# Performance work log

Measured on AMD Instinct MI355X. Metric: run time of the kernel, lower is better.

## Reference

```python
import jax, jax.numpy as jnp
import numpy as np

U_NODES, V_NODES, N_EDGES = 100000, 50000, 2000000
F_DIM, G_DIM, H_DIM = 32, 32, 8
G_HIDDEN = (64, 32)
F_HIDDEN = (64, 32)
OUT_DIM = 1


def _linear_params(key, din, dout):
    kw, kb = jax.random.split(key)
    lim = 1.0 / np.sqrt(din)
    w = jax.random.uniform(kw, (din, dout), jnp.float32, -lim, lim)
    b = jax.random.uniform(kb, (dout,), jnp.float32, -lim, lim)
    return w, b


def setup_inputs() -> dict:
    key = jax.random.key(0)
    ks = jax.random.split(key, 10)
    u = jax.random.normal(ks[0], (U_NODES, F_DIM), jnp.float32)
    v = jax.random.normal(ks[1], (V_NODES, G_DIM), jnp.float32)
    e_vals = jax.random.normal(ks[2], (N_EDGES, H_DIM), jnp.float32)
    e_src = jax.random.randint(ks[3], (N_EDGES,), 0, V_NODES, jnp.int32)  # V-side index (indices[0])
    e_dst = jax.random.randint(ks[4], (N_EDGES,), 0, U_NODES, jnp.int32)  # U-side index (indices[1])
    g_w1, g_b1 = _linear_params(ks[5], F_DIM + G_DIM + H_DIM, G_HIDDEN[0])
    g_w2, g_b2 = _linear_params(ks[6], G_HIDDEN[0], G_HIDDEN[1])
    f_w1, f_b1 = _linear_params(ks[7], F_DIM + G_HIDDEN[1], F_HIDDEN[0])
    f_w2, f_b2 = _linear_params(ks[8], F_HIDDEN[0], F_HIDDEN[1])
    t_w, t_b = _linear_params(ks[9], F_HIDDEN[1], OUT_DIM)
    return {
        "u": u, "v": v, "e_vals": e_vals, "e_src": e_src, "e_dst": e_dst,
        "g_w1": g_w1, "g_b1": g_b1, "g_w2": g_w2, "g_b2": g_b2,
        "f_w1": f_w1, "f_b1": f_b1, "f_w2": f_w2, "f_b2": f_b2,
        "t_w": t_w, "t_b": t_b,
    }


def reference(u, v, e_vals, e_src, e_dst,
              g_w1, g_b1, g_w2, g_b2,
              f_w1, f_b1, f_w2, f_b2,
              t_w, t_b):
    # gather edge endpoint features -> g MLP (two Linear+ReLU layers)
    edge_in = jnp.concatenate([u[e_dst], v[e_src], e_vals], axis=-1)  # (E, F+G+H)
    h = jax.nn.relu(edge_in @ g_w1 + g_b1)
    h = jax.nn.relu(h @ g_w2 + g_b2)  # (E, D)
    # torch.sparse.sum over dim=-3 (V axis) == segment-sum by the U index
    agg = jax.ops.segment_sum(h, e_dst, num_segments=u.shape[0])  # (U, D)
    # f MLP on concat([u, agg])
    z = jax.nn.relu(jnp.concatenate([u, agg], axis=-1) @ f_w1 + f_b1)
    z = jax.nn.relu(z @ f_w2 + f_b2)
    # tail linear (no relu) + sigmoid
    return jax.nn.sigmoid(z @ t_w + t_b)  # (U, 1)
```

## Files before the change

kernel.cpp:

```cpp
#include <hip/hip_runtime.h>
#include <cstdint>
#include <cstddef>

#define U_NODES 100000
#define V_NODES 50000
#define N_EDGES 2000000


typedef _Float16 f16x8 __attribute__((ext_vector_type(8)));
typedef _Float16 f16x2 __attribute__((ext_vector_type(2)));
typedef float    f32x4 __attribute__((ext_vector_type(4)));

__device__ __forceinline__ void load8f(const float* __restrict__ p, float* x) {
    const float4* p4 = reinterpret_cast<const float4*>(p);
    float4 a = p4[0], b = p4[1];
    x[0]=a.x; x[1]=a.y; x[2]=a.z; x[3]=a.w;
    x[4]=b.x; x[5]=b.y; x[6]=b.z; x[7]=b.w;
}

__device__ __forceinline__ void load32f(const float* __restrict__ p, float* x) {
    #pragma unroll
    for (int q = 0; q < 4; ++q) load8f(p + 8*q, x + 8*q);
}

__device__ __forceinline__ unsigned pack_bf16x2(float a, float b) {
    unsigned ua = __float_as_uint(a);
    ua = (ua + 0x7FFFu + ((ua >> 16) & 1u)) >> 16;
    unsigned ub = __float_as_uint(b);
    ub = (ub + 0x7FFFu + ((ub >> 16) & 1u)) & 0xFFFF0000u;
    return ua | ub;
}

__device__ __forceinline__ unsigned pk16(float a, float b) {
    union { f16x2 h; unsigned u; } c;
    c.h[0] = (_Float16)a; c.h[1] = (_Float16)b;
    return c.u;
}
__device__ __forceinline__ float f16lo(unsigned w) {
    union { unsigned short u; _Float16 h; } c; c.u = (unsigned short)(w & 0xFFFFu);
    return (float)c.h;
}
__device__ __forceinline__ float f16hi(unsigned w) {
    union { unsigned short u; _Float16 h; } c; c.u = (unsigned short)(w >> 16);
    return (float)c.h;
}
__device__ __forceinline__ f16x8 as_f16x8(uint4 x) {
    union { uint4 u; f16x8 h; } c; c.u = x; return c.h;
}


__global__ __launch_bounds__(256) void proj_u_kernel(
    const float* __restrict__ u, const float* __restrict__ g_w1,
    float* __restrict__ A)
{
    int n = blockIdx.x * 256 + threadIdx.x;
    if (n >= U_NODES) return;
    float x[32];
    load32f(u + (size_t)n * 32, x);
    float acc[64];
    #pragma unroll
    for (int j = 0; j < 64; ++j) acc[j] = 0.f;
    #pragma unroll
    for (int i = 0; i < 32; ++i) {
        #pragma unroll
        for (int j = 0; j < 64; ++j) acc[j] += x[i] * g_w1[i*64 + j];
    }
    float4* Ap = reinterpret_cast<float4*>(A + (size_t)n * 64);
    #pragma unroll
    for (int q = 0; q < 16; ++q)
        Ap[q] = make_float4(acc[4*q], acc[4*q+1], acc[4*q+2], acc[4*q+3]);
}

__global__ __launch_bounds__(256) void proj_v_kernel(
    const float* __restrict__ v, const float* __restrict__ g_w1,
    const float* __restrict__ g_b1, float* __restrict__ B)
{
    int n = blockIdx.x * 256 + threadIdx.x;
    if (n >= V_NODES) return;
    float x[32];
    load32f(v + (size_t)n * 32, x);
    float acc[64];
    #pragma unroll
    for (int j = 0; j < 64; ++j) acc[j] = g_b1[j];
    #pragma unroll
    for (int i = 0; i < 32; ++i) {
        #pragma unroll
        for (int j = 0; j < 64; ++j) acc[j] += x[i] * g_w1[(32+i)*64 + j];
    }
    float4* Bp = reinterpret_cast<float4*>(B + (size_t)n * 64);
    #pragma unroll
    for (int q = 0; q < 16; ++q)
        Bp[q] = make_float4(acc[4*q], acc[4*q+1], acc[4*q+2], acc[4*q+3]);
}


__global__ __launch_bounds__(256) void rank_kernel(
    const int* __restrict__ e_dst, int* __restrict__ deg, int* __restrict__ rank)
{
    int e = blockIdx.x * 256 + threadIdx.x;
    if (e >= N_EDGES) return;
    rank[e] = atomicAdd(&deg[e_dst[e]], 1);
}

__global__ __launch_bounds__(256) void scan_block_kernel(
    const int* __restrict__ deg, int* __restrict__ off, int* __restrict__ aux, int n)
{
    __shared__ int s[256];
    int tid = threadIdx.x;
    int i = blockIdx.x * 256 + tid;
    int x = (i < n) ? deg[i] : 0;
    s[tid] = x;
    __syncthreads();
    #pragma unroll
    for (int o = 1; o < 256; o <<= 1) {
        int t = (tid >= o) ? s[tid - o] : 0;
        __syncthreads();
        s[tid] += t;
        __syncthreads();
    }
    if (i < n) off[i + 1] = s[tid];
    if (tid == 255) aux[blockIdx.x] = s[255];
}

__global__ __launch_bounds__(512) void scan_aux_kernel(int* __restrict__ aux, int nA)
{
    __shared__ int s[512];
    int tid = threadIdx.x;
    int x = (tid < nA) ? aux[tid] : 0;
    s[tid] = x;
    __syncthreads();
    #pragma unroll
    for (int o = 1; o < 512; o <<= 1) {
        int t = (tid >= o) ? s[tid - o] : 0;
        __syncthreads();
        s[tid] += t;
        __syncthreads();
    }
    if (tid < nA) aux[tid] = s[tid] - x;
}

__global__ __launch_bounds__(256) void scan_add_kernel(
    int* __restrict__ off, const int* __restrict__ aux, int n)
{
    int i = blockIdx.x * 256 + threadIdx.x;
    if (i == 0) off[0] = 0;
    if (i < n) off[i + 1] += aux[i >> 8];
}

__global__ __launch_bounds__(256) void scatter_kernel(
    const int* __restrict__ e_dst, const int* __restrict__ off,
    const int* __restrict__ rank, int* __restrict__ sorted_eid)
{
    int e = blockIdx.x * 256 + threadIdx.x;
    if (e >= N_EDGES) return;
    int d = e_dst[e];
    sorted_eid[off[d] + rank[e]] = e;
}

__global__ __launch_bounds__(256) void permute_pack_kernel(
    const int* __restrict__ e_dst, const int* __restrict__ e_src,
    const int* __restrict__ rank, const int* __restrict__ off,
    const float* __restrict__ e_vals, unsigned* __restrict__ epk)
{
    int e = blockIdx.x * 256 + threadIdx.x;
    if (e >= N_EDGES) return;
    int d = e_dst[e];
    int pos = off[d] + rank[e];
    float ev[8];
    load8f(e_vals + (size_t)e * 8, ev);
    uint4 w0;
    w0.x = (unsigned)d;
    w0.y = (unsigned)e_src[e];
    w0.z = pk16(ev[0], ev[1]);
    w0.w = pk16(ev[2], ev[3]);
    uint2 w1;
    w1.x = pk16(ev[4], ev[5]);
    w1.y = pk16(ev[6], ev[7]);
    unsigned* dst = epk + (size_t)pos * 8;
    *reinterpret_cast<uint4*>(dst)     = w0;
    *reinterpret_cast<uint2*>(dst + 4) = w1;
}


template <bool HAS_A>
__global__ __launch_bounds__(256) void edge_mfma_kernel(
    const float* __restrict__ A, const float* __restrict__ B,
    const float* __restrict__ u, const unsigned* __restrict__ epk,
    const float* __restrict__ g_w1, const float* __restrict__ g_w2,
    const float* __restrict__ g_b2, float* __restrict__ agg)
{
    __shared__ unsigned s_h1[256 * 36];
    __shared__ unsigned s_w2[32 * 33];
    __shared__ int s_d[256];
    __shared__ int s_heads[256];
    __shared__ int s_cnt, s_prevd, s_nextd;

    const int tid = threadIdx.x;
    const long p = (long)blockIdx.x * 256 + tid;

    if (tid == 0) {
        s_cnt = 0;
        long pprev = (long)blockIdx.x * 256 - 1;
        s_prevd = (pprev < 0) ? -2 : (int)epk[(size_t)pprev * 8];
        long pnext = (long)blockIdx.x * 256 + 256;
        s_nextd = (pnext >= N_EDGES) ? -2 : (int)epk[(size_t)pnext * 8];
    }

    #pragma unroll
    for (int i = 0; i < 4; ++i) {
        int idx = tid + i * 256;
        int kp = idx >> 5, n = idx & 31;
        s_w2[kp * 33 + n] = pk16(g_w2[(2*kp)*32 + n], g_w2[(2*kp+1)*32 + n]);
    }

    int d = -1;
    if (p < N_EDGES) {
        const unsigned* ep = epk + (size_t)p * 8;
        uint4 w0 = *reinterpret_cast<const uint4*>(ep);
        uint2 w1 = *reinterpret_cast<const uint2*>(ep + 4);
        d = (int)w0.x;
        int s = (int)w0.y;

        float h1[64];
        if constexpr (HAS_A) {
            const float4* Ap = reinterpret_cast<const float4*>(A + (size_t)d * 64);
            #pragma unroll
            for (int q = 0; q < 16; ++q) {
                float4 a = Ap[q];
                h1[4*q+0] = a.x; h1[4*q+1] = a.y; h1[4*q+2] = a.z; h1[4*q+3] = a.w;
            }
        } else {
            #pragma unroll
            for (int j = 0; j < 64; ++j) h1[j] = 0.f;
            float x[32];
            load32f(u + (size_t)d * 32, x);
            #pragma unroll
            for (int i = 0; i < 32; ++i) {
                #pragma unroll
                for (int j = 0; j < 64; ++j) h1[j] += x[i] * g_w1[i*64 + j];
            }
        }
        {
            const float4* Bp = reinterpret_cast<const float4*>(B + (size_t)s * 64);
            #pragma unroll
            for (int q = 0; q < 16; ++q) {
                float4 b = Bp[q];
                h1[4*q+0] += b.x; h1[4*q+1] += b.y; h1[4*q+2] += b.z; h1[4*q+3] += b.w;
            }
        }
        float ev[8];
        ev[0]=f16lo(w0.z); ev[1]=f16hi(w0.z); ev[2]=f16lo(w0.w); ev[3]=f16hi(w0.w);
        ev[4]=f16lo(w1.x); ev[5]=f16hi(w1.x); ev[6]=f16lo(w1.y); ev[7]=f16hi(w1.y);
        #pragma unroll
        for (int i = 0; i < 8; ++i) {
            #pragma unroll
            for (int j = 0; j < 64; ++j) h1[j] += ev[i] * g_w1[(64+i)*64 + j];
        }
        #pragma unroll
        for (int j = 0; j < 64; ++j) h1[j] = fmaxf(h1[j], 0.f);

        #pragma unroll
        for (int q = 0; q < 8; ++q) {
            uint4 w;
            w.x = pk16(h1[8*q+0], h1[8*q+1]);
            w.y = pk16(h1[8*q+2], h1[8*q+3]);
            w.z = pk16(h1[8*q+4], h1[8*q+5]);
            w.w = pk16(h1[8*q+6], h1[8*q+7]);
            *reinterpret_cast<uint4*>(&s_h1[tid*36 + 4*q]) = w;
        }
    }
    s_d[tid] = d;
    __syncthreads();

    if (p < N_EDGES) {
        int prevd = (tid == 0) ? s_prevd : s_d[tid - 1];
        bool true_head = (prevd != d);
        bool is_head = (tid == 0) || true_head;
        if (is_head) {
            int idx = atomicAdd(&s_cnt, 1);
            s_heads[idx] = tid | (true_head ? 0x10000 : 0);
        }
    }

    const int lane = tid & 63;
    const int wb   = (tid >> 6) * 64;
    const int lg   = lane >> 4;
    const int lm   = lane & 15;

    f32x4 acc[4][2];
    #pragma unroll
    for (int mt = 0; mt < 4; ++mt) {
        #pragma unroll
        for (int nt = 0; nt < 2; ++nt) {
            acc[mt][nt][0] = 0.f; acc[mt][nt][1] = 0.f;
            acc[mt][nt][2] = 0.f; acc[mt][nt][3] = 0.f;
        }
    }
    #pragma unroll
    for (int kt = 0; kt < 2; ++kt) {
        uint4 bf0, bf1;
        {
            int kp = kt*16 + lg*4;
            bf0.x = s_w2[(kp+0)*33 + lm];      bf1.x = s_w2[(kp+0)*33 + 16 + lm];
            bf0.y = s_w2[(kp+1)*33 + lm];      bf1.y = s_w2[(kp+1)*33 + 16 + lm];
            bf0.z = s_w2[(kp+2)*33 + lm];      bf1.z = s_w2[(kp+2)*33 + 16 + lm];
            bf0.w = s_w2[(kp+3)*33 + lm];      bf1.w = s_w2[(kp+3)*33 + 16 + lm];
        }
        f16x8 b0 = as_f16x8(bf0), b1 = as_f16x8(bf1);
        #pragma unroll
        for (int mt = 0; mt < 4; ++mt) {
            uint4 av = *reinterpret_cast<const uint4*>(
                &s_h1[(wb + mt*16 + lm)*36 + kt*16 + lg*4]);
            f16x8 a = as_f16x8(av);
            acc[mt][0] = __builtin_amdgcn_mfma_f32_16x16x32_f16(a, b0, acc[mt][0], 0, 0, 0);
            acc[mt][1] = __builtin_amdgcn_mfma_f32_16x16x32_f16(a, b1, acc[mt][1], 0, 0, 0);
        }
    }
    float b2a = g_b2[lm];
    float b2b = g_b2[16 + lm];
    __syncthreads();

    float* h2f = reinterpret_cast<float*>(s_h1);
    #pragma unroll
    for (int mt = 0; mt < 4; ++mt) {
        #pragma unroll
        for (int r = 0; r < 4; ++r) {
            int row = wb + mt*16 + lg*4 + r;
            h2f[row*36 + lm]      = fmaxf(acc[mt][0][r] + b2a, 0.f);
            h2f[row*36 + 16 + lm] = fmaxf(acc[mt][1][r] + b2b, 0.f);
        }
    }
    __syncthreads();

    const int nseg = s_cnt;
    const int next_d = s_nextd;
    for (int w = tid; w < nseg * 16; w += 256) {
        int seg = w >> 4, cp = w & 15;
        int ent = s_heads[seg];
        int h = ent & 0xFFFF;
        bool thead = (ent & 0x10000) != 0;
        int dd = s_d[h];
        float s0 = 0.f, s1 = 0.f;
        int r = h;
        while (r < 256 && s_d[r] == dd) {
            s0 += h2f[r*36 + 2*cp];
            s1 += h2f[r*36 + 2*cp + 1];
            ++r;
        }
        bool end_complete = (r < 256) || (next_d != dd);
        float* dst = agg + (size_t)dd * 32 + 2 * cp;
        if (thead && end_complete) {
            *reinterpret_cast<float2*>(dst) = make_float2(s0, s1);
        } else {
            atomicAdd(dst + 0, s0);
            atomicAdd(dst + 1, s1);
        }
    }
}


template <bool HAS_A, bool HAS_B>
__global__ __launch_bounds__(256) void edge_sorted_kernel(
    const float* __restrict__ A, const float* __restrict__ B,
    const float* __restrict__ u, const float* __restrict__ v,
    const float* __restrict__ e_vals, const int* __restrict__ e_src,
    const int* __restrict__ e_dst, const int* __restrict__ seid,
    const float* __restrict__ g_w1, const float* __restrict__ g_b1,
    const float* __restrict__ g_w2, const float* __restrict__ g_b2,
    float* __restrict__ agg)
{
    __shared__ unsigned lds_h[256][17];
    __shared__ int lds_d[256];
    __shared__ int lds_heads[256];
    __shared__ int lds_cnt;
    __shared__ int lds_prev_d, lds_next_d;

    const int tid = threadIdx.x;
    const long p = (long)blockIdx.x * 256 + tid;

    if (tid == 0) {
        lds_cnt = 0;
        long pprev = (long)blockIdx.x * 256 - 1;
        lds_prev_d = (pprev < 0) ? -2 : e_dst[seid[pprev]];
        long pnext = (long)blockIdx.x * 256 + 256;
        lds_next_d = (pnext >= N_EDGES) ? -2 : e_dst[seid[pnext]];
    }

    int d = -1;
    if (p < N_EDGES) {
        int eid = seid[p];
        d = e_dst[eid];
        int s = e_src[eid];

        float h1[64];
        if constexpr (HAS_A) {
            const float4* Ap = reinterpret_cast<const float4*>(A + (size_t)d * 64);
            #pragma unroll
            for (int q = 0; q < 16; ++q) {
                float4 a = Ap[q];
                h1[4*q+0] = a.x; h1[4*q+1] = a.y; h1[4*q+2] = a.z; h1[4*q+3] = a.w;
            }
        } else {
            #pragma unroll
            for (int j = 0; j < 64; ++j) h1[j] = 0.f;
            float x[32];
            load32f(u + (size_t)d * 32, x);
            #pragma unroll
            for (int i = 0; i < 32; ++i) {
                #pragma unroll
                for (int j = 0; j < 64; ++j) h1[j] += x[i] * g_w1[i*64 + j];
            }
        }
        if constexpr (HAS_B) {
            const float4* Bp = reinterpret_cast<const float4*>(B + (size_t)s * 64);
            #pragma unroll
            for (int q = 0; q < 16; ++q) {
                float4 b = Bp[q];
                h1[4*q+0] += b.x; h1[4*q+1] += b.y; h1[4*q+2] += b.z; h1[4*q+3] += b.w;
            }
        } else {
            #pragma unroll
            for (int j = 0; j < 64; ++j) h1[j] += g_b1[j];
            float x[32];
            load32f(v + (size_t)s * 32, x);
            #pragma unroll
            for (int i = 0; i < 32; ++i) {
                #pragma unroll
                for (int j = 0; j < 64; ++j) h1[j] += x[i] * g_w1[(32+i)*64 + j];
            }
        }
        float ev[8];
        load8f(e_vals + (size_t)eid * 8, ev);
        #pragma unroll
        for (int i = 0; i < 8; ++i) {
            #pragma unroll
            for (int j = 0; j < 64; ++j) h1[j] += ev[i] * g_w1[(64+i)*64 + j];
        }
        #pragma unroll
        for (int j = 0; j < 64; ++j) h1[j] = fmaxf(h1[j], 0.f);

        float h2[32];
        #pragma unroll
        for (int k = 0; k < 32; ++k) h2[k] = g_b2[k];
        #pragma unroll
        for (int i = 0; i < 64; ++i) {
            #pragma unroll
            for (int k = 0; k < 32; ++k) h2[k] += h1[i] * g_w2[i*32 + k];
        }
        #pragma unroll
        for (int cp = 0; cp < 16; ++cp)
            lds_h[tid][cp] = pack_bf16x2(fmaxf(h2[2*cp], 0.f), fmaxf(h2[2*cp+1], 0.f));
    }
    lds_d[tid] = d;
    __syncthreads();

    if (p < N_EDGES) {
        int prevd = (tid == 0) ? lds_prev_d : lds_d[tid - 1];
        bool true_head = (prevd != d);
        bool is_head = (tid == 0) || true_head;
        if (is_head) {
            int idx = atomicAdd(&lds_cnt, 1);
            lds_heads[idx] = tid | (true_head ? 0x10000 : 0);
        }
    }
    __syncthreads();

    const int nseg = lds_cnt;
    const int next_d = lds_next_d;
    for (int w = tid; w < nseg * 16; w += 256) {
        int seg = w >> 4, cp = w & 15;
        int ent = lds_heads[seg];
        int h = ent & 0xFFFF;
        bool thead = (ent & 0x10000) != 0;
        int dd = lds_d[h];
        float s0 = 0.f, s1 = 0.f;
        int r = h;
        while (r < 256 && lds_d[r] == dd) {
            unsigned x = lds_h[r][cp];
            s0 += __uint_as_float(x << 16);
            s1 += __uint_as_float(x & 0xFFFF0000u);
            ++r;
        }
        bool end_complete = (r < 256) || (next_d != dd);
        float* dst = agg + (size_t)dd * 32 + 2 * cp;
        if (thead && end_complete) {
            *reinterpret_cast<float2*>(dst) = make_float2(s0, s1);
        } else {
            atomicAdd(dst + 0, s0);
            atomicAdd(dst + 1, s1);
        }
    }
}


__global__ __launch_bounds__(256) void node_kernel(
    const float* __restrict__ u, const float* __restrict__ agg,
    const float* __restrict__ f_w1, const float* __restrict__ f_b1,
    const float* __restrict__ f_w2, const float* __restrict__ f_b2,
    const float* __restrict__ t_w, const float* __restrict__ t_b,
    float* __restrict__ out)
{
    int n = blockIdx.x * 256 + threadIdx.x;
    if (n >= U_NODES) return;
    float x[64];
    load32f(u   + (size_t)n * 32, x);
    load32f(agg + (size_t)n * 32, x + 32);
    float z1[64];
    #pragma unroll
    for (int j = 0; j < 64; ++j) z1[j] = f_b1[j];
    #pragma unroll
    for (int i = 0; i < 64; ++i) {
        #pragma unroll
        for (int j = 0; j < 64; ++j) z1[j] += x[i] * f_w1[i*64 + j];
    }
    #pragma unroll
    for (int j = 0; j < 64; ++j) z1[j] = fmaxf(z1[j], 0.f);
    float z2[32];
    #pragma unroll
    for (int k = 0; k < 32; ++k) z2[k] = f_b2[k];
    #pragma unroll
    for (int j = 0; j < 64; ++j) {
        #pragma unroll
        for (int k = 0; k < 32; ++k) z2[k] += z1[j] * f_w2[j*32 + k];
    }
    #pragma unroll
    for (int k = 0; k < 32; ++k) z2[k] = fmaxf(z2[k], 0.f);
    float o = t_b[0];
    #pragma unroll
    for (int k = 0; k < 32; ++k) o += z2[k] * t_w[k];
    out[n] = 1.f / (1.f + expf(-o));
}


__global__ __launch_bounds__(256) void edge_direct_kernel(
    const float* __restrict__ u, const float* __restrict__ v,
    const float* __restrict__ e_vals, const int* __restrict__ e_src,
    const int* __restrict__ e_dst, const float* __restrict__ g_w1,
    const float* __restrict__ g_b1, const float* __restrict__ g_w2,
    const float* __restrict__ g_b2, float* __restrict__ agg)
{
    int e = blockIdx.x * 256 + threadIdx.x;
    if (e >= N_EDGES) return;
    int d = e_dst[e];
    int s = e_src[e];
    float x[72];
    load32f(u + (size_t)d * 32, x);
    load32f(v + (size_t)s * 32, x + 32);
    load8f(e_vals + (size_t)e * 8, x + 64);
    float h1[64];
    #pragma unroll
    for (int j = 0; j < 64; ++j) h1[j] = g_b1[j];
    #pragma unroll
    for (int i = 0; i < 72; ++i) {
        #pragma unroll
        for (int j = 0; j < 64; ++j) h1[j] += x[i] * g_w1[i*64 + j];
    }
    #pragma unroll
    for (int j = 0; j < 64; ++j) h1[j] = fmaxf(h1[j], 0.f);
    float acc2[32];
    #pragma unroll
    for (int k = 0; k < 32; ++k) acc2[k] = g_b2[k];
    #pragma unroll
    for (int i = 0; i < 64; ++i) {
        #pragma unroll
        for (int k = 0; k < 32; ++k) acc2[k] += h1[i] * g_w2[i*32 + k];
    }
    float* aggp = agg + (size_t)d * 32;
    #pragma unroll
    for (int k = 0; k < 32; ++k) atomicAdd(aggp + k, fmaxf(acc2[k], 0.f));
}


static inline size_t align256(size_t x) { return (x + 255) & ~(size_t)255; }

extern "C" void kernel_launch(void* const* d_in, const int* in_sizes, int n_in,
                              void* d_out, int out_size, void* d_ws, size_t ws_size,
                              hipStream_t stream) {
    const float* u      = (const float*)d_in[0];
    const float* v      = (const float*)d_in[1];
    const float* e_vals = (const float*)d_in[2];
    const int*   e_src  = (const int*)  d_in[3];
    const int*   e_dst  = (const int*)  d_in[4];
    const float* g_w1   = (const float*)d_in[5];
    const float* g_b1   = (const float*)d_in[6];
    const float* g_w2   = (const float*)d_in[7];
    const float* g_b2   = (const float*)d_in[8];
    const float* f_w1   = (const float*)d_in[9];
    const float* f_b1   = (const float*)d_in[10];
    const float* f_w2   = (const float*)d_in[11];
    const float* f_b2   = (const float*)d_in[12];
    const float* t_w    = (const float*)d_in[13];
    const float* t_b    = (const float*)d_in[14];
    float* out = (float*)d_out;

    char* wsc = (char*)d_ws;
    const int nChunks = (U_NODES + 255) / 256;
    const int eBlocks = (N_EDGES + 255) / 256;

    const size_t degB  = align256((size_t)U_NODES * 4);
    const size_t offB  = align256((size_t)(U_NODES + 1) * 4);
    const size_t auxB  = align256((size_t)nChunks * 4);
    const size_t aggB  = align256((size_t)U_NODES * 32 * 4);
    const size_t e4B   = align256((size_t)N_EDGES * 4);
    const size_t epkB  = align256((size_t)N_EDGES * 32);
    const size_t bB    = align256((size_t)V_NODES * 64 * 4);
    const size_t aB    = align256((size_t)U_NODES * 64 * 4);

    size_t o = 0;
    size_t oDeg = o; o += degB;
    size_t oOff = o; o += offB;
    size_t oAux = o; o += auxB;
    size_t oAgg = o; o += aggB;
    size_t baseNeed = o;

    size_t oEp = o;  o += epkB;
    size_t oBn = o;  o += bB;
    size_t needT2r = o + e4B;
    size_t oAn = o;  o += aB;
    size_t needT1 = o;

    size_t o3 = baseNeed;
    size_t oSeid = o3; o3 += e4B;
    size_t needT4 = o3 + e4B;
    size_t oB3 = o3;   o3 += bB;
    size_t oA3 = o3;   o3 += aB;
    size_t needT3 = o3;

    int* deg   = (int*)(wsc + oDeg);
    int* off   = (int*)(wsc + oOff);
    int* aux   = (int*)(wsc + oAux);
    float* agg = (float*)(wsc + oAgg);

    if (ws_size >= needT2r) {
        const bool hasA = (ws_size >= needT1);
        unsigned* epk = (unsigned*)(wsc + oEp);
        float* B   = (float*)(wsc + oBn);
        float* A   = hasA ? (float*)(wsc + oAn) : nullptr;
        int* rank  = hasA ? (int*)A : (int*)(wsc + oAn);

        hipMemsetAsync(deg, 0, (size_t)U_NODES * 4, stream);
        hipMemsetAsync(agg, 0, (size_t)U_NODES * 32 * 4, stream);

        rank_kernel<<<eBlocks, 256, 0, stream>>>(e_dst, deg, rank);
        scan_block_kernel<<<nChunks, 256, 0, stream>>>(deg, off, aux, U_NODES);
        scan_aux_kernel<<<1, 512, 0, stream>>>(aux, nChunks);
        scan_add_kernel<<<nChunks, 256, 0, stream>>>(off, aux, U_NODES);
        permute_pack_kernel<<<eBlocks, 256, 0, stream>>>(e_dst, e_src, rank, off,
                                                         e_vals, epk);
        proj_v_kernel<<<(V_NODES + 255) / 256, 256, 0, stream>>>(v, g_w1, g_b1, B);
        if (hasA) {
            proj_u_kernel<<<(U_NODES + 255) / 256, 256, 0, stream>>>(u, g_w1, A);
            edge_mfma_kernel<true><<<eBlocks, 256, 0, stream>>>(
                A, B, u, epk, g_w1, g_w2, g_b2, agg);
        } else {
            edge_mfma_kernel<false><<<eBlocks, 256, 0, stream>>>(
                nullptr, B, u, epk, g_w1, g_w2, g_b2, agg);
        }
        node_kernel<<<(U_NODES + 255) / 256, 256, 0, stream>>>(
            u, agg, f_w1, f_b1, f_w2, f_b2, t_w, t_b, out);
    } else if (ws_size >= needT4) {
        const bool hasAB = (ws_size >= needT3);
        int* seid = (int*)(wsc + oSeid);
        float* B = hasAB ? (float*)(wsc + oB3) : nullptr;
        float* A = hasAB ? (float*)(wsc + oA3) : nullptr;
        int* rank = hasAB ? (int*)A : (int*)(wsc + oSeid + e4B);

        hipMemsetAsync(deg, 0, (size_t)U_NODES * 4, stream);
        hipMemsetAsync(agg, 0, (size_t)U_NODES * 32 * 4, stream);

        rank_kernel<<<eBlocks, 256, 0, stream>>>(e_dst, deg, rank);
        scan_block_kernel<<<nChunks, 256, 0, stream>>>(deg, off, aux, U_NODES);
        scan_aux_kernel<<<1, 512, 0, stream>>>(aux, nChunks);
        scan_add_kernel<<<nChunks, 256, 0, stream>>>(off, aux, U_NODES);
        scatter_kernel<<<eBlocks, 256, 0, stream>>>(e_dst, off, rank, seid);

        if (hasAB) {
            proj_v_kernel<<<(V_NODES + 255) / 256, 256, 0, stream>>>(v, g_w1, g_b1, B);
            proj_u_kernel<<<(U_NODES + 255) / 256, 256, 0, stream>>>(u, g_w1, A);
            edge_sorted_kernel<true, true><<<eBlocks, 256, 0, stream>>>(
                A, B, u, v, e_vals, e_src, e_dst, seid, g_w1, g_b1, g_w2, g_b2, agg);
        } else {
            edge_sorted_kernel<false, false><<<eBlocks, 256, 0, stream>>>(
                nullptr, nullptr, u, v, e_vals, e_src, e_dst, seid,
                g_w1, g_b1, g_w2, g_b2, agg);
        }
        node_kernel<<<(U_NODES + 255) / 256, 256, 0, stream>>>(
            u, agg, f_w1, f_b1, f_w2, f_b2, t_w, t_b, out);
    } else {
        float* agg0 = (float*)wsc;
        hipMemsetAsync(agg0, 0, (size_t)U_NODES * 32 * 4, stream);
        edge_direct_kernel<<<eBlocks, 256, 0, stream>>>(
            u, v, e_vals, e_src, e_dst, g_w1, g_b1, g_w2, g_b2, agg0);
        node_kernel<<<(U_NODES + 255) / 256, 256, 0, stream>>>(
            u, agg0, f_w1, f_b1, f_w2, f_b2, t_w, t_b, out);
    }
}
```

Baseline: 422.5 us.

## Replace per-node counting sort with 64-node bucket sort and block-local aggregation

Replaces the per-destination atomic rank, full U-sized scan and permute with a coarse bucket sort: 64-node buckets are histogrammed in shared memory per 1024-thread block, then packed in block-local order. The edge kernel now runs one block per bucket, computes the first layer per-lane with fdot2 for the edge features, runs layer two on MFMA, and accumulates into shared-memory agg with LDS atomics before one coalesced write. This removes global atomics, the agg memset and the segment-head logic. In exchange, bucket sizes vary, each block's loop length depends on its edge count, and shared-memory atomic contention rises on hot nodes.

```diff
diff --git a/kernel.cpp b/kernel.cpp
--- a/kernel.cpp
+++ b/kernel.cpp
@@ -5,6 +5,13 @@
 #define U_NODES 100000
 #define V_NODES 50000
 #define N_EDGES 2000000
+#define UBLKS ((U_NODES + 255) / 256)
+#define VBLKS ((V_NODES + 255) / 256)
+
+#define BNODES 64
+#define NBUK ((U_NODES + BNODES - 1) / BNODES)
+#define HB 128
+#define EPB ((N_EDGES + HB - 1) / HB)
 
 
 typedef _Float16 f16x8 __attribute__((ext_vector_type(8)));
@@ -48,6 +55,15 @@
     union { uint4 u; f16x8 h; } c; c.u = x; return c.h;
 }
 
+__device__ __forceinline__ float fdot2f(unsigned a, unsigned b, float c) {
+#if defined(__has_builtin) && __has_builtin(__builtin_amdgcn_fdot2)
+    union { unsigned u; f16x2 h; } ca, cb; ca.u = a; cb.u = b;
+    return __builtin_amdgcn_fdot2(ca.h, cb.h, c, false);
+#else
+    return c + f16lo(a)*f16lo(b) + f16hi(a)*f16hi(b);
+#endif
+}
+
 
 __global__ __launch_bounds__(256) void proj_u_kernel(
     const float* __restrict__ u, const float* __restrict__ g_w1,
@@ -94,12 +110,23 @@
 }
 
 
-__global__ __launch_bounds__(256) void rank_kernel(
-    const int* __restrict__ e_dst, int* __restrict__ deg, int* __restrict__ rank)
-{
-    int e = blockIdx.x * 256 + threadIdx.x;
-    if (e >= N_EDGES) return;
-    rank[e] = atomicAdd(&deg[e_dst[e]], 1);
+__global__ __launch_bounds__(1024) void bucket_hist_kernel(
+    const int* __restrict__ e_dst, int* __restrict__ bucketcnt,
+    int* __restrict__ blockbase)
+{
+    __shared__ int hist[NBUK];
+    const int tid = threadIdx.x, blk = blockIdx.x;
+    for (int i = tid; i < NBUK; i += 1024) hist[i] = 0;
+    __syncthreads();
+    int e0 = blk * EPB;
+    int e1 = e0 + EPB; if (e1 > N_EDGES) e1 = N_EDGES;
+    for (int e = e0 + tid; e < e1; e += 1024)
+        atomicAdd(&hist[e_dst[e] >> 6], 1);
+    __syncthreads();
+    for (int b = tid; b < NBUK; b += 1024) {
+        int c = hist[b];
+        blockbase[blk * NBUK + b] = c ? atomicAdd(&bucketcnt[b], c) : 0;
+    }
 }
 
 __global__ __launch_bounds__(256) void scan_block_kernel(
@@ -147,64 +174,79 @@
     if (i < n) off[i + 1] += aux[i >> 8];
 }
 
-__global__ __launch_bounds__(256) void scatter_kernel(
-    const int* __restrict__ e_dst, const int* __restrict__ off,
-    const int* __restrict__ rank, int* __restrict__ sorted_eid)
-{
-    int e = blockIdx.x * 256 + threadIdx.x;
-    if (e >= N_EDGES) return;
-    int d = e_dst[e];
-    sorted_eid[off[d] + rank[e]] = e;
-}
-
-__global__ __launch_bounds__(256) void permute_pack_kernel(
+__global__ __launch_bounds__(1024) void bucket_pack_kernel(
     const int* __restrict__ e_dst, const int* __restrict__ e_src,
-    const int* __restrict__ rank, const int* __restrict__ off,
-    const float* __restrict__ e_vals, unsigned* __restrict__ epk)
-{
-    int e = blockIdx.x * 256 + threadIdx.x;
-    if (e >= N_EDGES) return;
-    int d = e_dst[e];
-    int pos = off[d] + rank[e];
-    float ev[8];
-    load8f(e_vals + (size_t)e * 8, ev);
-    uint4 w0;
-    w0.x = (unsigned)d;
-    w0.y = (unsigned)e_src[e];
-    w0.z = pk16(ev[0], ev[1]);
-    w0.w = pk16(ev[2], ev[3]);
-    uint2 w1;
-    w1.x = pk16(ev[4], ev[5]);
-    w1.y = pk16(ev[6], ev[7]);
-    unsigned* dst = epk + (size_t)pos * 8;
-    *reinterpret_cast<uint4*>(dst)     = w0;
-    *reinterpret_cast<uint2*>(dst + 4) = w1;
-}
-
-
-template <bool HAS_A>
-__global__ __launch_bounds__(256) void edge_mfma_kernel(
+    const float* __restrict__ e_vals, const int* __restrict__ bucket_off,
+    const int* __restrict__ blockbase, unsigned* __restrict__ epk)
+{
+    __shared__ int cur[NBUK];
+    __shared__ int base[NBUK];
+    const int tid = threadIdx.x, blk = blockIdx.x;
+    for (int i = tid; i < NBUK; i += 1024) {
+        cur[i] = 0;
+        base[i] = bucket_off[i] + blockbase[blk * NBUK + i];
+    }
+    __syncthreads();
+    int e0 = blk * EPB;
+    int e1 = e0 + EPB; if (e1 > N_EDGES) e1 = N_EDGES;
+    for (int e = e0 + tid; e < e1; e += 1024) {
+        int d = e_dst[e];
+        int b = d >> 6;
+        int lr = atomicAdd(&cur[b], 1);
+        int pos = base[b] + lr;
+        float ev[8];
+        load8f(e_vals + (size_t)e * 8, ev);
+        uint4 w0;
+        w0.x = (unsigned)d;
+        w0.y = (unsigned)e_src[e];
+        w0.z = pk16(ev[0], ev[1]);
+        w0.w = pk16(ev[2], ev[3]);
+        uint2 w1;
+        w1.x = pk16(ev[4], ev[5]);
+        w1.y = pk16(ev[6], ev[7]);
+        unsigned* dst = epk + (size_t)pos * 8;
+        *reinterpret_cast<uint4*>(dst)     = w0;
+        *reinterpret_cast<uint2*>(dst + 4) = w1;
+    }
+}
+
+
+__device__ __forceinline__ void load_recs_b(
+    const unsigned* __restrict__ epk, int beg, int cnt, int t, int wv, int lm,
+    int* dM, int* sM, unsigned (*evp)[4])
+{
+    #pragma unroll
+    for (int mt = 0; mt < 4; ++mt) {
+        int rel = t*256 + wv*64 + mt*16 + lm;
+        if (rel < cnt) {
+            const unsigned* ep = epk + (size_t)(beg + rel) * 8;
+            uint4 w0 = *reinterpret_cast<const uint4*>(ep);
+            uint2 w1 = *reinterpret_cast<const uint2*>(ep + 4);
+            dM[mt] = (int)w0.x; sM[mt] = (int)w0.y;
+            evp[mt][0] = w0.z; evp[mt][1] = w0.w; evp[mt][2] = w1.x; evp[mt][3] = w1.y;
+        } else {
+            dM[mt] = -1; sM[mt] = 0;
+            evp[mt][0] = evp[mt][1] = evp[mt][2] = evp[mt][3] = 0;
+        }
+    }
+}
+
+__global__ __launch_bounds__(256) void edge_agg_kernel(
     const float* __restrict__ A, const float* __restrict__ B,
-    const float* __restrict__ u, const unsigned* __restrict__ epk,
+    const unsigned* __restrict__ epk, const int* __restrict__ bucket_off,
     const float* __restrict__ g_w1, const float* __restrict__ g_w2,
     const float* __restrict__ g_b2, float* __restrict__ agg)
 {
-    __shared__ unsigned s_h1[256 * 36];
+    __shared__ float s_agg[BNODES * 33];
     __shared__ unsigned s_w2[32 * 33];
-    __shared__ int s_d[256];
-    __shared__ int s_heads[256];
-    __shared__ int s_cnt, s_prevd, s_nextd;
+    __shared__ __align__(16) unsigned s_w1e[4 * 64];
+    __shared__ int s_dl[2][256];
 
     const int tid = threadIdx.x;
-    const long p = (long)blockIdx.x * 256 + tid;
-
-    if (tid == 0) {
-        s_cnt = 0;
-        long pprev = (long)blockIdx.x * 256 - 1;
-        s_prevd = (pprev < 0) ? -2 : (int)epk[(size_t)pprev * 8];
-        long pnext = (long)blockIdx.x * 256 + 256;
-        s_nextd = (pnext >= N_EDGES) ? -2 : (int)epk[(size_t)pnext * 8];
-    }
+    const int bk  = blockIdx.x;
+    const int beg = bucket_off[bk];
+    const int cnt = bucket_off[bk + 1] - beg;
+    const int node0 = bk * BNODES;
 
     #pragma unroll
     for (int i = 0; i < 4; ++i) {
@@ -212,152 +254,183 @@
         int kp = idx >> 5, n = idx & 31;
         s_w2[kp * 33 + n] = pk16(g_w2[(2*kp)*32 + n], g_w2[(2*kp+1)*32 + n]);
     }
-
-    int d = -1;
-    if (p < N_EDGES) {
-        const unsigned* ep = epk + (size_t)p * 8;
-        uint4 w0 = *reinterpret_cast<const uint4*>(ep);
-        uint2 w1 = *reinterpret_cast<const uint2*>(ep + 4);
-        d = (int)w0.x;
-        int s = (int)w0.y;
-
-        float h1[64];
-        if constexpr (HAS_A) {
-            const float4* Ap = reinterpret_cast<const float4*>(A + (size_t)d * 64);
-            #pragma unroll
-            for (int q = 0; q < 16; ++q) {
-                float4 a = Ap[q];
-                h1[4*q+0] = a.x; h1[4*q+1] = a.y; h1[4*q+2] = a.z; h1[4*q+3] = a.w;
-            }
-        } else {
-            #pragma unroll
-            for (int j = 0; j < 64; ++j) h1[j] = 0.f;
-            float x[32];
-            load32f(u + (size_t)d * 32, x);
-            #pragma unroll
-            for (int i = 0; i < 32; ++i) {
+    {
+        int i2 = tid >> 6, c = tid & 63;
+        s_w1e[i2 * 64 + c] = pk16(g_w1[(64 + 2*i2)*64 + c], g_w1[(64 + 2*i2 + 1)*64 + c]);
+    }
+    for (int i = tid; i < BNODES * 33; i += 256) s_agg[i] = 0.f;
+
+    const int wv   = tid >> 6;
+    const int lane = tid & 63;
+    const int lm   = lane & 15;
+    const int lg   = lane >> 4;
+    const float b2a = g_b2[lm], b2b = g_b2[16 + lm];
+
+    const int nt = (cnt + 255) >> 8;
+    int dC[4], sC[4]; unsigned evC[4][4];
+    if (nt > 0) load_recs_b(epk, beg, cnt, 0, wv, lm, dC, sC, evC);
+    __syncthreads();
+
+    for (int t = 0; t < nt; ++t) {
+        uint4 afr[4][2];
+        #pragma unroll
+        for (int kt = 0; kt < 2; ++kt) {
+            float acc[4][8];
+            #pragma unroll
+            for (int mt = 0; mt < 4; ++mt) {
+                if (dC[mt] >= 0) {
+                    const float4* Ap = reinterpret_cast<const float4*>(A + (size_t)dC[mt]*64 + kt*32 + lg*8);
+                    const float4* Bp = reinterpret_cast<const float4*>(B + (size_t)sC[mt]*64 + kt*32 + lg*8);
+                    float4 a0 = Ap[0], a1 = Ap[1], b0 = Bp[0], b1 = Bp[1];
+                    acc[mt][0] = a0.x + b0.x; acc[mt][1] = a0.y + b0.y;
+                    acc[mt][2] = a0.z + b0.z; acc[mt][3] = a0.w + b0.w;
+                    acc[mt][4] = a1.x + b1.x; acc[mt][5] = a1.y + b1.y;
+                    acc[mt][6] = a1.z + b1.z; acc[mt][7] = a1.w + b1.w;
+                } else {
+                    #pragma unroll
+                    for (int j = 0; j < 8; ++j) acc[mt][j] = 0.f;
+                }
+            }
+            #pragma unroll
+            for (int i2 = 0; i2 < 4; ++i2) {
+                uint4 wA = *reinterpret_cast<const uint4*>(&s_w1e[i2*64 + kt*32 + lg*8]);
+                uint4 wB = *reinterpret_cast<const uint4*>(&s_w1e[i2*64 + kt*32 + lg*8 + 4]);
                 #pragma unroll
-                for (int j = 0; j < 64; ++j) h1[j] += x[i] * g_w1[i*64 + j];
-            }
-        }
-        {
-            const float4* Bp = reinterpret_cast<const float4*>(B + (size_t)s * 64);
-            #pragma unroll
-            for (int q = 0; q < 16; ++q) {
-                float4 b = Bp[q];
-                h1[4*q+0] += b.x; h1[4*q+1] += b.y; h1[4*q+2] += b.z; h1[4*q+3] += b.w;
-            }
-        }
-        float ev[8];
-        ev[0]=f16lo(w0.z); ev[1]=f16hi(w0.z); ev[2]=f16lo(w0.w); ev[3]=f16hi(w0.w);
-        ev[4]=f16lo(w1.x); ev[5]=f16hi(w1.x); ev[6]=f16lo(w1.y); ev[7]=f16hi(w1.y);
-        #pragma unroll
-        for (int i = 0; i < 8; ++i) {
-            #pragma unroll
-            for (int j = 0; j < 64; ++j) h1[j] += ev[i] * g_w1[(64+i)*64 + j];
-        }
-        #pragma unroll
-        for (int j = 0; j < 64; ++j) h1[j] = fmaxf(h1[j], 0.f);
-
-        #pragma unroll
-        for (int q = 0; q < 8; ++q) {
-            uint4 w;
-            w.x = pk16(h1[8*q+0], h1[8*q+1]);
-            w.y = pk16(h1[8*q+2], h1[8*q+3]);
-            w.z = pk16(h1[8*q+4], h1[8*q+5]);
-            w.w = pk16(h1[8*q+6], h1[8*q+7]);
-            *reinterpret_cast<uint4*>(&s_h1[tid*36 + 4*q]) = w;
-        }
-    }
-    s_d[tid] = d;
-    __syncthreads();
-
-    if (p < N_EDGES) {
-        int prevd = (tid == 0) ? s_prevd : s_d[tid - 1];
-        bool true_head = (prevd != d);
-        bool is_head = (tid == 0) || true_head;
-        if (is_head) {
-            int idx = atomicAdd(&s_cnt, 1);
-            s_heads[idx] = tid | (true_head ? 0x10000 : 0);
-        }
-    }
-
-    const int lane = tid & 63;
-    const int wb   = (tid >> 6) * 64;
-    const int lg   = lane >> 4;
-    const int lm   = lane & 15;
-
-    f32x4 acc[4][2];
-    #pragma unroll
-    for (int mt = 0; mt < 4; ++mt) {
-        #pragma unroll
-        for (int nt = 0; nt < 2; ++nt) {
-            acc[mt][nt][0] = 0.f; acc[mt][nt][1] = 0.f;
-            acc[mt][nt][2] = 0.f; acc[mt][nt][3] = 0.f;
-        }
-    }
-    #pragma unroll
-    for (int kt = 0; kt < 2; ++kt) {
-        uint4 bf0, bf1;
-        {
+                for (int mt = 0; mt < 4; ++mt) {
+                    unsigned e2 = evC[mt][i2];
+                    acc[mt][0] = fdot2f(e2, wA.x, acc[mt][0]);
+                    acc[mt][1] = fdot2f(e2, wA.y, acc[mt][1]);
+                    acc[mt][2] = fdot2f(e2, wA.z, acc[mt][2]);
+                    acc[mt][3] = fdot2f(e2, wA.w, acc[mt][3]);
+                    acc[mt][4] = fdot2f(e2, wB.x, acc[mt][4]);
+                    acc[mt][5] = fdot2f(e2, wB.y, acc[mt][5]);
+                    acc[mt][6] = fdot2f(e2, wB.z, acc[mt][6]);
+                    acc[mt][7] = fdot2f(e2, wB.w, acc[mt][7]);
+                }
+            }
+            #pragma unroll
+            for (int mt = 0; mt < 4; ++mt) {
+                uint4 w;
+                w.x = pk16(fmaxf(acc[mt][0], 0.f), fmaxf(acc[mt][1], 0.f));
+                w.y = pk16(fmaxf(acc[mt][2], 0.f), fmaxf(acc[mt][3], 0.f));
+                w.z = pk16(fmaxf(acc[mt][4], 0.f), fmaxf(acc[mt][5], 0.f));
+                w.w = pk16(fmaxf(acc[mt][6], 0.f), fmaxf(acc[mt][7], 0.f));
+                afr[mt][kt] = w;
+            }
+        }
+
+        f32x4 mac[4][2];
+        #pragma unroll
+        for (int mt = 0; mt < 4; ++mt) {
+            #pragma unroll
+            for (int nt2 = 0; nt2 < 2; ++nt2) {
+                mac[mt][nt2][0] = 0.f; mac[mt][nt2][1] = 0.f;
+                mac[mt][nt2][2] = 0.f; mac[mt][nt2][3] = 0.f;
+            }
+        }
+        #pragma unroll
+        for (int kt = 0; kt < 2; ++kt) {
+            uint4 bf0, bf1;
             int kp = kt*16 + lg*4;
             bf0.x = s_w2[(kp+0)*33 + lm];      bf1.x = s_w2[(kp+0)*33 + 16 + lm];
             bf0.y = s_w2[(kp+1)*33 + lm];      bf1.y = s_w2[(kp+1)*33 + 16 + lm];
             bf0.z = s_w2[(kp+2)*33 + lm];      bf1.z = s_w2[(kp+2)*33 + 16 + lm];
             bf0.w = s_w2[(kp+3)*33 + lm];      bf1.w = s_w2[(kp+3)*33 + 16 + lm];
-        }
-        f16x8 b0 = as_f16x8(bf0), b1 = as_f16x8(bf1);
+            f16x8 b0 = as_f16x8(bf0), b1 = as_f16x8(bf1);
+            #pragma unroll
+            for (int mt = 0; mt < 4; ++mt) {
+                f16x8 a = as_f16x8(afr[mt][kt]);
+                mac[mt][0] = __builtin_amdgcn_mfma_f32_16x16x32_f16(a, b0, mac[mt][0], 0, 0, 0);
+                mac[mt][1] = __builtin_amdgcn_mfma_f32_16x16x32_f16(a, b1, mac[mt][1], 0, 0, 0);
+            }
+        }
+
+        if (lg == 0) {
+            #pragma unroll
+            for (int mt = 0; mt < 4; ++mt) s_dl[t & 1][wv*64 + mt*16 + lm] = dC[mt];
+        }
+        __syncthreads();
+
+        if (t + 1 < nt) load_recs_b(epk, beg, cnt, t + 1, wv, lm, dC, sC, evC);
+
         #pragma unroll
         for (int mt = 0; mt < 4; ++mt) {
-            uint4 av = *reinterpret_cast<const uint4*>(
-                &s_h1[(wb + mt*16 + lm)*36 + kt*16 + lg*4]);
-            f16x8 a = as_f16x8(av);
-            acc[mt][0] = __builtin_amdgcn_mfma_f32_16x16x32_f16(a, b0, acc[mt][0], 0, 0, 0);
-            acc[mt][1] = __builtin_amdgcn_mfma_f32_16x16x32_f16(a, b1, acc[mt][1], 0, 0, 0);
-        }
-    }
-    float b2a = g_b2[lm];
-    float b2b = g_b2[16 + lm];
-    __syncthreads();
-
-    float* h2f = reinterpret_cast<float*>(s_h1);
-    #pragma unroll
-    for (int mt = 0; mt < 4; ++mt) {
-        #pragma unroll
-        for (int r = 0; r < 4; ++r) {
-            int row = wb + mt*16 + lg*4 + r;
-            h2f[row*36 + lm]      = fmaxf(acc[mt][0][r] + b2a, 0.f);
-            h2f[row*36 + 16 + lm] = fmaxf(acc[mt][1][r] + b2b, 0.f);
-        }
-    }
-    __syncthreads();
-
-    const int nseg = s_cnt;
-    const int next_d = s_nextd;
-    for (int w = tid; w < nseg * 16; w += 256) {
-        int seg = w >> 4, cp = w & 15;
-        int ent = s_heads[seg];
-        int h = ent & 0xFFFF;
-        bool thead = (ent & 0x10000) != 0;
-        int dd = s_d[h];
-        float s0 = 0.f, s1 = 0.f;
-        int r = h;
-        while (r < 256 && s_d[r] == dd) {
-            s0 += h2f[r*36 + 2*cp];
-            s1 += h2f[r*36 + 2*cp + 1];
-            ++r;
-        }
-        bool end_complete = (r < 256) || (next_d != dd);
-        float* dst = agg + (size_t)dd * 32 + 2 * cp;
-        if (thead && end_complete) {
-            *reinterpret_cast<float2*>(dst) = make_float2(s0, s1);
-        } else {
-            atomicAdd(dst + 0, s0);
-            atomicAdd(dst + 1, s1);
-        }
-    }
-}
-
+            #pragma unroll
+            for (int r = 0; r < 4; ++r) {
+                int dd = s_dl[t & 1][wv*64 + mt*16 + lg*4 + r];
+                if (dd >= 0) {
+                    int loc = (dd & (BNODES - 1)) * 33;
+                    atomicAdd(&s_agg[loc + lm],      fmaxf(mac[mt][0][r] + b2a, 0.f));
+                    atomicAdd(&s_agg[loc + 16 + lm], fmaxf(mac[mt][1][r] + b2b, 0.f));
+                }
+            }
+        }
+    }
+    __syncthreads();
+
+    for (int i = tid; i < BNODES * 32; i += 256) {
+        int n = node0 + (i >> 5);
+        if (n < U_NODES) agg[(size_t)n * 32 + (i & 31)] = s_agg[(i >> 5) * 33 + (i & 31)];
+    }
+}
+
+
+__global__ __launch_bounds__(256) void node_kernel(
+    const float* __restrict__ u, const float* __restrict__ agg,
+    const float* __restrict__ f_w1, const float* __restrict__ f_b1,
+    const float* __restrict__ f_w2, const float* __restrict__ f_b2,
+    const float* __restrict__ t_w, const float* __restrict__ t_b,
+    float* __restrict__ out)
+{
+    int n = blockIdx.x * 256 + threadIdx.x;
+    if (n >= U_NODES) return;
+    float x[64];
+    load32f(u   + (size_t)n * 32, x);
+    load32f(agg + (size_t)n * 32, x + 32);
+    float z1[64];
+    #pragma unroll
+    for (int j = 0; j < 64; ++j) z1[j] = f_b1[j];
+    #pragma unroll
+    for (int i = 0; i < 64; ++i) {
+        #pragma unroll
+        for (int j = 0; j < 64; ++j) z1[j] += x[i] * f_w1[i*64 + j];
+    }
+    #pragma unroll
+    for (int j = 0; j < 64; ++j) z1[j] = fmaxf(z1[j], 0.f);
+    float z2[32];
+    #pragma unroll
+    for (int k = 0; k < 32; ++k) z2[k] = f_b2[k];
+    #pragma unroll
+    for (int j = 0; j < 64; ++j) {
+        #pragma unroll
+        for (int k = 0; k < 32; ++k) z2[k] += z1[j] * f_w2[j*32 + k];
+    }
+    #pragma unroll
+    for (int k = 0; k < 32; ++k) z2[k] = fmaxf(z2[k], 0.f);
+    float o = t_b[0];
+    #pragma unroll
+    for (int k = 0; k < 32; ++k) o += z2[k] * t_w[k];
+    out[n] = 1.f / (1.f + expf(-o));
+}
+
+
+__global__ __launch_bounds__(256) void rank_kernel(
+    const int* __restrict__ e_dst, int* __restrict__ deg, int* __restrict__ rank)
+{
+    int e = blockIdx.x * 256 + threadIdx.x;
+    if (e >= N_EDGES) return;
+    rank[e] = atomicAdd(&deg[e_dst[e]], 1);
+}
+
+__global__ __launch_bounds__(256) void scatter_kernel(
+    const int* __restrict__ e_dst, const int* __restrict__ off,
+    const int* __restrict__ rank, int* __restrict__ sorted_eid)
+{
+    int e = blockIdx.x * 256 + threadIdx.x;
+    if (e >= N_EDGES) return;
+    int d = e_dst[e];
+    sorted_eid[off[d] + rank[e]] = e;
+}
 
 template <bool HAS_A, bool HAS_B>
 __global__ __launch_bounds__(256) void edge_sorted_kernel(
@@ -491,46 +564,6 @@
         }
     }
 }
-
-
-__global__ __launch_bounds__(256) void node_kernel(
-    const float* __restrict__ u, const float* __restrict__ agg,
-    const float* __restrict__ f_w1, const float* __restrict__ f_b1,
-    const float* __restrict__ f_w2, const float* __restrict__ f_b2,
-    const float* __restrict__ t_w, const float* __restrict__ t_b,
-    float* __restrict__ out)
-{
-    int n = blockIdx.x * 256 + threadIdx.x;
-    if (n >= U_NODES) return;
-    float x[64];
-    load32f(u   + (size_t)n * 32, x);
-    load32f(agg + (size_t)n * 32, x + 32);
-    float z1[64];
-    #pragma unroll
-    for (int j = 0; j < 64; ++j) z1[j] = f_b1[j];
-    #pragma unroll
-    for (int i = 0; i < 64; ++i) {
-        #pragma unroll
-        for (int j = 0; j < 64; ++j) z1[j] += x[i] * f_w1[i*64 + j];
-    }
-    #pragma unroll
-    for (int j = 0; j < 64; ++j) z1[j] = fmaxf(z1[j], 0.f);
-    float z2[32];
-    #pragma unroll
-    for (int k = 0; k < 32; ++k) z2[k] = f_b2[k];
-    #pragma unroll
-    for (int j = 0; j < 64; ++j) {
-        #pragma unroll
-        for (int k = 0; k < 32; ++k) z2[k] += z1[j] * f_w2[j*32 + k];
-    }
-    #pragma unroll
-    for (int k = 0; k < 32; ++k) z2[k] = fmaxf(z2[k], 0.f);
-    float o = t_b[0];
-    #pragma unroll
-    for (int k = 0; k < 32; ++k) o += z2[k] * t_w[k];
-    out[n] = 1.f / (1.f + expf(-o));
-}
-
 
 __global__ __launch_bounds__(256) void edge_direct_kernel(
     const float* __restrict__ u, const float* __restrict__ v,
@@ -594,73 +627,76 @@
     float* out = (float*)d_out;
 
     char* wsc = (char*)d_ws;
-    const int nChunks = (U_NODES + 255) / 256;
     const int eBlocks = (N_EDGES + 255) / 256;
-
-    const size_t degB  = align256((size_t)U_NODES * 4);
-    const size_t offB  = align256((size_t)(U_NODES + 1) * 4);
-    const size_t auxB  = align256((size_t)nChunks * 4);
+    const int nChunksB = (NBUK + 255) / 256;
+
+    const size_t bcB   = align256((size_t)NBUK * 4);
+    const size_t boB   = align256((size_t)(NBUK + 1) * 4);
+    const size_t auxB  = align256((size_t)nChunksB * 4);
+    const size_t bbB   = align256((size_t)HB * NBUK * 4);
     const size_t aggB  = align256((size_t)U_NODES * 32 * 4);
-    const size_t e4B   = align256((size_t)N_EDGES * 4);
     const size_t epkB  = align256((size_t)N_EDGES * 32);
     const size_t bB    = align256((size_t)V_NODES * 64 * 4);
     const size_t aB    = align256((size_t)U_NODES * 64 * 4);
+    const size_t e4B   = align256((size_t)N_EDGES * 4);
 
     size_t o = 0;
-    size_t oDeg = o; o += degB;
-    size_t oOff = o; o += offB;
+    size_t oBc  = o; o += bcB;
+    size_t oBo  = o; o += boB;
     size_t oAux = o; o += auxB;
+    size_t oBb  = o; o += bbB;
     size_t oAgg = o; o += aggB;
-    size_t baseNeed = o;
-
-    size_t oEp = o;  o += epkB;
-    size_t oBn = o;  o += bB;
-    size_t needT2r = o + e4B;
-    size_t oAn = o;  o += aB;
-    size_t needT1 = o;
-
-    size_t o3 = baseNeed;
+    size_t oEp  = o; o += epkB;
+    size_t oBn  = o; o += bB;
+    size_t oAn  = o; o += aB;
+    size_t needNew = o;
+
+    const size_t degB = align256((size_t)U_NODES * 4);
+    const size_t offB = align256((size_t)(U_NODES + 1) * 4);
+    const int nChunksU = (U_NODES + 255) / 256;
+    const size_t auxUB = align256((size_t)nChunksU * 4);
+    size_t o3 = 0;
+    size_t oDeg3 = o3; o3 += degB;
+    size_t oOff3 = o3; o3 += offB;
+    size_t oAux3 = o3; o3 += auxUB;
+    size_t oAgg3 = o3; o3 += aggB;
     size_t oSeid = o3; o3 += e4B;
     size_t needT4 = o3 + e4B;
     size_t oB3 = o3;   o3 += bB;
     size_t oA3 = o3;   o3 += aB;
     size_t needT3 = o3;
 
-    int* deg   = (int*)(wsc + oDeg);
-    int* off   = (int*)(wsc + oOff);
-    int* aux   = (int*)(wsc + oAux);
-    float* agg = (float*)(wsc + oAgg);
-
-    if (ws_size >= needT2r) {
-        const bool hasA = (ws_size >= needT1);
-        unsigned* epk = (unsigned*)(wsc + oEp);
-        float* B   = (float*)(wsc + oBn);
-        float* A   = hasA ? (float*)(wsc + oAn) : nullptr;
-        int* rank  = hasA ? (int*)A : (int*)(wsc + oAn);
-
-        hipMemsetAsync(deg, 0, (size_t)U_NODES * 4, stream);
-        hipMemsetAsync(agg, 0, (size_t)U_NODES * 32 * 4, stream);
-
-        rank_kernel<<<eBlocks, 256, 0, stream>>>(e_dst, deg, rank);
-        scan_block_kernel<<<nChunks, 256, 0, stream>>>(deg, off, aux, U_NODES);
-        scan_aux_kernel<<<1, 512, 0, stream>>>(aux, nChunks);
-        scan_add_kernel<<<nChunks, 256, 0, stream>>>(off, aux, U_NODES);
-        permute_pack_kernel<<<eBlocks, 256, 0, stream>>>(e_dst, e_src, rank, off,
-                                                         e_vals, epk);
-        proj_v_kernel<<<(V_NODES + 255) / 256, 256, 0, stream>>>(v, g_w1, g_b1, B);
-        if (hasA) {
-            proj_u_kernel<<<(U_NODES + 255) / 256, 256, 0, stream>>>(u, g_w1, A);
-            edge_mfma_kernel<true><<<eBlocks, 256, 0, stream>>>(
-                A, B, u, epk, g_w1, g_w2, g_b2, agg);
-        } else {
-            edge_mfma_kernel<false><<<eBlocks, 256, 0, stream>>>(
-                nullptr, B, u, epk, g_w1, g_w2, g_b2, agg);
-        }
-        node_kernel<<<(U_NODES + 255) / 256, 256, 0, stream>>>(
+    if (ws_size >= needNew) {
+        int* bucketcnt = (int*)(wsc + oBc);
+        int* bucketoff = (int*)(wsc + oBo);
+        int* aux       = (int*)(wsc + oAux);
+        int* blockbase = (int*)(wsc + oBb);
+        float* agg     = (float*)(wsc + oAgg);
+        unsigned* epk  = (unsigned*)(wsc + oEp);
+        float* B       = (float*)(wsc + oBn);
+        float* A       = (float*)(wsc + oAn);
+
+        hipMemsetAsync(bucketcnt, 0, (size_t)NBUK * 4, stream);
+
+        bucket_hist_kernel<<<HB, 1024, 0, stream>>>(e_dst, bucketcnt, blockbase);
+        scan_block_kernel<<<nChunksB, 256, 0, stream>>>(bucketcnt, bucketoff, aux, NBUK);
+        scan_aux_kernel<<<1, 512, 0, stream>>>(aux, nChunksB);
+        scan_add_kernel<<<nChunksB, 256, 0, stream>>>(bucketoff, aux, NBUK);
+        bucket_pack_kernel<<<HB, 1024, 0, stream>>>(e_dst, e_src, e_vals,
+                                                    bucketoff, blockbase, epk);
+        proj_v_kernel<<<VBLKS, 256, 0, stream>>>(v, g_w1, g_b1, B);
+        proj_u_kernel<<<UBLKS, 256, 0, stream>>>(u, g_w1, A);
+        edge_agg_kernel<<<NBUK, 256, 0, stream>>>(A, B, epk, bucketoff,
+                                                  g_w1, g_w2, g_b2, agg);
+        node_kernel<<<UBLKS, 256, 0, stream>>>(
             u, agg, f_w1, f_b1, f_w2, f_b2, t_w, t_b, out);
     } else if (ws_size >= needT4) {
         const bool hasAB = (ws_size >= needT3);
-        int* seid = (int*)(wsc + oSeid);
+        int* deg   = (int*)(wsc + oDeg3);
+        int* off   = (int*)(wsc + oOff3);
+        int* aux   = (int*)(wsc + oAux3);
+        float* agg = (float*)(wsc + oAgg3);
+        int* seid  = (int*)(wsc + oSeid);
         float* B = hasAB ? (float*)(wsc + oB3) : nullptr;
         float* A = hasAB ? (float*)(wsc + oA3) : nullptr;
         int* rank = hasAB ? (int*)A : (int*)(wsc + oSeid + e4B);
@@ -669,14 +705,14 @@
         hipMemsetAsync(agg, 0, (size_t)U_NODES * 32 * 4, stream);
 
         rank_kernel<<<eBlocks, 256, 0, stream>>>(e_dst, deg, rank);
-        scan_block_kernel<<<nChunks, 256, 0, stream>>>(deg, off, aux, U_NODES);
-        scan_aux_kernel<<<1, 512, 0, stream>>>(aux, nChunks);
-        scan_add_kernel<<<nChunks, 256, 0, stream>>>(off, aux, U_NODES);
+        scan_block_kernel<<<nChunksU, 256, 0, stream>>>(deg, off, aux, U_NODES);
+        scan_aux_kernel<<<1, 512, 0, stream>>>(aux, nChunksU);
+        scan_add_kernel<<<nChunksU, 256, 0, stream>>>(off, aux, U_NODES);
         scatter_kernel<<<eBlocks, 256, 0, stream>>>(e_dst, off, rank, seid);
 
         if (hasAB) {
-            proj_v_kernel<<<(V_NODES + 255) / 256, 256, 0, stream>>>(v, g_w1, g_b1, B);
-            proj_u_kernel<<<(U_NODES + 255) / 256, 256, 0, stream>>>(u, g_w1, A);
+            proj_v_kernel<<<VBLKS, 256, 0, stream>>>(v, g_w1, g_b1, B);
+            proj_u_kernel<<<UBLKS, 256, 0, stream>>>(u, g_w1, A);
             edge_sorted_kernel<true, true><<<eBlocks, 256, 0, stream>>>(
                 A, B, u, v, e_vals, e_src, e_dst, seid, g_w1, g_b1, g_w2, g_b2, agg);
         } else {
@@ -684,14 +720,14 @@
                 nullptr, nullptr, u, v, e_vals, e_src, e_dst, seid,
                 g_w1, g_b1, g_w2, g_b2, agg);
         }
-        node_kernel<<<(U_NODES + 255) / 256, 256, 0, stream>>>(
+        node_kernel<<<UBLKS, 256, 0, stream>>>(
             u, agg, f_w1, f_b1, f_w2, f_b2, t_w, t_b, out);
     } else {
         float* agg0 = (float*)wsc;
         hipMemsetAsync(agg0, 0, (size_t)U_NODES * 32 * 4, stream);
         edge_direct_kernel<<<eBlocks, 256, 0, stream>>>(
             u, v, e_vals, e_src, e_dst, g_w1, g_b1, g_w2, g_b2, agg0);
-        node_kernel<<<(U_NODES + 255) / 256, 256, 0, stream>>>(
+        node_kernel<<<UBLKS, 256, 0, stream>>>(
             u, agg0, f_w1, f_b1, f_w2, f_b2, t_w, t_b, out);
     }
 }
```

Result: slower. 629.3 us (+49.0%).
